# Kernel tuning notes

Hardware: AMD Instinct MI355X
Metric: run time of the kernel (lower is better)

Reference implementation:

```python
import jax, jax.numpy as jnp
import numpy as np

# normalization module stand-ins (simple monotone scalings, as in the repo they
# are fixed elementwise rescalings of the raw quantities)
def norm_local_x(n):
    return n

def norm_unit_contraction(c):
    return c

def norm_local_N(N):
    return jnp.log1p(N.astype(jnp.float32))

norm_TNG_radii = norm_local_x
norm_local_v = norm_local_x
norm_local_v0 = norm_local_x

EPS = 1e-5


def setup_inputs() -> dict:
    key = jax.random.key(0)
    ks = jax.random.split(key, 12)
    B, T, ND, KB = 2, 1024, 256, 3
    K_IN, H, L = 19, 128, 128
    x0 = 0.3 * jax.random.normal(ks[0], (B, T, 3), dtype=jnp.float32)
    # DM positions in local frame, |x| must stay < 1.05 (assert in original)
    x = jax.random.uniform(ks[1], (B, T, ND, 3), dtype=jnp.float32) - 0.5
    N = jax.random.randint(ks[2], (B, T), 1, 512, dtype=jnp.int32)
    basis = jax.random.normal(ks[3], (B, KB, 3), dtype=jnp.float32)
    v = jax.random.normal(ks[4], (B, T, ND, 3), dtype=jnp.float32)
    P200c = 0.5 + jax.random.uniform(ks[5], (B,), dtype=jnp.float32)
    s = 0.1
    W0 = s * jax.random.normal(ks[6], (K_IN, H - 1), dtype=jnp.float32)
    b0 = jnp.zeros((H - 1,), jnp.float32)
    W1 = s * jax.random.normal(ks[7], (H, H), dtype=jnp.float32)
    b1 = jnp.zeros((H,), jnp.float32)
    W2 = s * jax.random.normal(ks[8], (H, L), dtype=jnp.float32)
    b2 = jnp.zeros((L,), jnp.float32)
    return {"x0": x0, "x": x, "N": N, "basis": basis, "v": v, "P200c": P200c,
            "W0": W0, "b0": b0, "W1": W1, "b1": b1, "W2": W2, "b2": b2}


def create_scalars(x0, x, N, basis, v):
    B, T, ND, _ = x.shape
    # velocities relative to local mean (halo -> local frame)
    v0 = jnp.mean(v, axis=2)                      # [B,T,3]
    vc = v - v0[:, :, None, :]                    # [B,T,ND,3]

    x_norm = jnp.linalg.norm(x, axis=-1, keepdims=True) + EPS     # [B,T,ND,1]
    xu = x / x_norm
    x0_norm = jnp.linalg.norm(x0, axis=-1, keepdims=True) + EPS   # [B,T,1]
    x0u = x0 / x0_norm
    v0_norm = jnp.linalg.norm(v0, axis=-1, keepdims=True) + EPS   # [B,T,1]
    v0u = v0 / v0_norm
    v_norm = jnp.linalg.norm(vc, axis=-1, keepdims=True) + EPS    # [B,T,ND,1]
    vu = vc / v_norm

    bc = lambda a: jnp.broadcast_to(a[:, :, None, :], (B, T, ND, a.shape[-1]))

    feats = [
        norm_local_x(x_norm),                                          # |x| [1]
        norm_unit_contraction(jnp.einsum('btnd,bkd->btnk', xu, basis)),# x.basis [3]
        jnp.broadcast_to(norm_local_N(N)[:, :, None, None], (B, T, ND, 1)),  # N [1]
        bc(norm_TNG_radii(x0_norm)),                                   # |x0| [1]
        bc(norm_unit_contraction(jnp.einsum('btd,bkd->btk', x0u, basis))),  # x0.basis [3]
        bc(norm_local_v0(v0_norm)),                                    # |v0| [1]
        bc(norm_unit_contraction(jnp.einsum('btd,bkd->btk', v0u, basis))),  # v0.basis [3]
        bc(norm_unit_contraction(jnp.sum(x0u * v0u, axis=-1, keepdims=True))),  # x0.v0 [1]
        norm_local_v(v_norm),                                          # |v| [1]
        norm_unit_contraction(jnp.einsum('btnd,bkd->btnk', vu, basis)),# v.basis [3]
        norm_unit_contraction(jnp.sum(xu * vu, axis=-1, keepdims=True)),  # x.v [1]
    ]
    return jnp.concatenate(feats, axis=-1)  # [B,T,ND,19]


def reference(x0, x, N, basis, v, P200c, W0, b0, W1, b1, W2, b2):
    scalars = create_scalars(x0, x, N, basis, v)          # [B,T,ND,19]
    h = jax.nn.leaky_relu(scalars @ W0 + b0)              # [B,T,ND,H-1]
    h = jnp.mean(h, axis=2)                               # pool -> [B,T,H-1]
    h = jnp.concatenate([h, norm_local_N(N)[..., None]], axis=-1)  # [B,T,H]
    h = jax.nn.leaky_relu(h @ W1 + b1)                    # [B,T,H]
    out = h @ W2 + b2                                     # [B,T,Nlatent]
    return (1.0 / P200c)[:, None, None] * out
```

## Files before the change

kernel.cpp:

```cpp
#include <hip/hip_runtime.h>
#include <hip/hip_bf16.h>
#include <math.h>

#define EPSV 1e-5f
#define HD   128
#define AROW 40
#define WROW 40

typedef __attribute__((ext_vector_type(8))) short bf16x8;
typedef __attribute__((ext_vector_type(4))) float f32x4;

__global__ __launch_bounds__(256, 2) void net_fused(
    const float* __restrict__ x0g, const float* __restrict__ xg,
    const int*   __restrict__ Ng,  const float* __restrict__ basisg,
    const float* __restrict__ vg,  const float* __restrict__ Pg,
    const float* __restrict__ W0,  const float* __restrict__ b0,
    const float* __restrict__ W1,  const float* __restrict__ b1,
    const float* __restrict__ W2,  const float* __restrict__ b2,
    float* __restrict__ out, int Tn, int NDn)
{
    __shared__ __align__(16) __hip_bfloat16 SA[256 * AROW];
    __shared__ __align__(16) __hip_bfloat16 Wt1[128 * WROW];
    __shared__ __align__(16) __hip_bfloat16 Wt2[128 * WROW];
    __shared__ float cvec[HD];
    __shared__ float part[4][HD];
    __shared__ float hvec[HD];
    __shared__ float h1vec[HD];
    __shared__ float tailred[2][HD];
    __shared__ float vred[4][3];

    const int bt   = blockIdx.x;
    const int b    = bt / Tn;
    const int tid  = threadIdx.x;
    const int lane = tid & 63;
    const int wave = tid >> 6;

    const long pbase = ((long)bt * NDn + tid) * 3;
    const float xi0 = xg[pbase+0], xi1 = xg[pbase+1], xi2 = xg[pbase+2];
    const float vi0 = vg[pbase+0], vi1 = vg[pbase+1], vi2 = vg[pbase+2];

    float s0 = vi0, s1 = vi1, s2 = vi2;
    #pragma unroll
    for (int off = 32; off > 0; off >>= 1) {
        s0 += __shfl_down(s0, off);
        s1 += __shfl_down(s1, off);
        s2 += __shfl_down(s2, off);
    }
    if (lane == 0) { vred[wave][0] = s0; vred[wave][1] = s1; vred[wave][2] = s2; }

    {
        const int RV[9] = {0, 1, 2, 3, 14, 15, 16, 17, 18};
        if (tid < 128) {
            const int n = tid;
            __hip_bfloat16* w1 = &Wt1[n * WROW];
            __hip_bfloat16* w2 = &Wt2[n * WROW];
            const __hip_bfloat16 z16 = __float2bfloat16(0.0f);
            #pragma unroll
            for (int kk = 0; kk < 9; ++kk) {
                const float wv = (n < 127) ? W0[RV[kk] * 127 + n] : 0.0f;
                const __hip_bfloat16 hi = __float2bfloat16(wv);
                const __hip_bfloat16 lo = __float2bfloat16(wv - __bfloat162float(hi));
                w1[kk] = hi;  w1[16 + kk] = hi;
                w2[kk] = lo;  w2[16 + kk] = lo;
            }
            #pragma unroll
            for (int kk = 9; kk < 16; ++kk) {
                w1[kk] = z16;  w1[kk + 16] = z16;
                w2[kk] = z16;  w2[kk + 16] = z16;
            }
        }
    }
    __syncthreads();

    const float inv_nd = 1.0f / (float)NDn;
    const float v00 = (vred[0][0]+vred[1][0]+vred[2][0]+vred[3][0]) * inv_nd;
    const float v01 = (vred[0][1]+vred[1][1]+vred[2][1]+vred[3][1]) * inv_nd;
    const float v02 = (vred[0][2]+vred[1][2]+vred[2][2]+vred[3][2]) * inv_nd;

    const float p0 = x0g[bt*3+0], p1 = x0g[bt*3+1], p2 = x0g[bt*3+2];
    float bas[3][3];
    #pragma unroll
    for (int k = 0; k < 3; ++k)
        #pragma unroll
        for (int c = 0; c < 3; ++c)
            bas[k][c] = basisg[(b*3 + k)*3 + c];

    const float x0n  = sqrtf(p0*p0 + p1*p1 + p2*p2) + EPSV;
    const float ix0n = 1.0f / x0n;
    const float x0u0 = p0*ix0n, x0u1 = p1*ix0n, x0u2 = p2*ix0n;

    const float v0n  = sqrtf(v00*v00 + v01*v01 + v02*v02) + EPSV;
    const float iv0n = 1.0f / v0n;
    const float v0u0 = v00*iv0n, v0u1 = v01*iv0n, v0u2 = v02*iv0n;

    const float logN = log1pf((float)Ng[bt]);

    if (tid < 128) {
        float c = 0.0f;
        if (tid < 127) {
            float fc[10];
            fc[0] = logN;
            fc[1] = x0n;
            fc[2] = x0u0*bas[0][0] + x0u1*bas[0][1] + x0u2*bas[0][2];
            fc[3] = x0u0*bas[1][0] + x0u1*bas[1][1] + x0u2*bas[1][2];
            fc[4] = x0u0*bas[2][0] + x0u1*bas[2][1] + x0u2*bas[2][2];
            fc[5] = v0n;
            fc[6] = v0u0*bas[0][0] + v0u1*bas[0][1] + v0u2*bas[0][2];
            fc[7] = v0u0*bas[1][0] + v0u1*bas[1][1] + v0u2*bas[1][2];
            fc[8] = v0u0*bas[2][0] + v0u1*bas[2][1] + v0u2*bas[2][2];
            fc[9] = x0u0*v0u0 + x0u1*v0u1 + x0u2*v0u2;
            c = b0[tid];
            #pragma unroll
            for (int i = 0; i < 10; ++i)
                c = fmaf(fc[i], W0[(4 + i) * 127 + tid], c);
        }
        cvec[tid] = c;
    }

    {
        const float xn  = sqrtf(xi0*xi0 + xi1*xi1 + xi2*xi2) + EPSV;
        const float ixn = 1.0f / xn;
        const float xu0 = xi0*ixn, xu1 = xi1*ixn, xu2 = xi2*ixn;

        const float c0 = vi0 - v00, c1 = vi1 - v01, c2 = vi2 - v02;
        const float vn  = sqrtf(c0*c0 + c1*c1 + c2*c2) + EPSV;
        const float ivn = 1.0f / vn;
        const float vu0 = c0*ivn, vu1 = c1*ivn, vu2 = c2*ivn;

        float f[9];
        f[0] = xn;
        f[1] = xu0*bas[0][0] + xu1*bas[0][1] + xu2*bas[0][2];
        f[2] = xu0*bas[1][0] + xu1*bas[1][1] + xu2*bas[1][2];
        f[3] = xu0*bas[2][0] + xu1*bas[2][1] + xu2*bas[2][2];
        f[4] = vn;
        f[5] = vu0*bas[0][0] + vu1*bas[0][1] + vu2*bas[0][2];
        f[6] = vu0*bas[1][0] + vu1*bas[1][1] + vu2*bas[1][2];
        f[7] = vu0*bas[2][0] + vu1*bas[2][1] + vu2*bas[2][2];
        f[8] = xu0*vu0 + xu1*vu1 + xu2*vu2;

        __hip_bfloat16* Ar = &SA[tid * AROW];
        const __hip_bfloat16 z16 = __float2bfloat16(0.0f);
        #pragma unroll
        for (int kk = 0; kk < 9; ++kk) {
            const __hip_bfloat16 hi = __float2bfloat16(f[kk]);
            Ar[kk]      = hi;
            Ar[16 + kk] = __float2bfloat16(f[kk] - __bfloat162float(hi));
        }
        #pragma unroll
        for (int kk = 9; kk < 16; ++kk) {
            Ar[kk]      = z16;
            Ar[kk + 16] = z16;
        }
    }
    __syncthreads();

    {
        const int quad = lane >> 4;
        const int lm   = lane & 15;

        bf16x8 bf1[8], bf2[8];
        float  cl[8];
        #pragma unroll
        for (int nt = 0; nt < 8; ++nt) {
            bf1[nt] = *reinterpret_cast<const bf16x8*>(&Wt1[(nt*16 + lm) * WROW + quad*8]);
            bf2[nt] = *reinterpret_cast<const bf16x8*>(&Wt2[(nt*16 + lm) * WROW + quad*8]);
            cl[nt]  = cvec[nt*16 + lm];
        }

        float pooled[8];
        #pragma unroll
        for (int nt = 0; nt < 8; ++nt) pooled[nt] = 0.0f;

        const f32x4 zero = {0.f, 0.f, 0.f, 0.f};
        #pragma unroll
        for (int mt = 0; mt < 4; ++mt) {
            const int particle = wave*64 + mt*16 + lm;
            const bf16x8 af = *reinterpret_cast<const bf16x8*>(&SA[particle * AROW + quad*8]);
            #pragma unroll
            for (int nt = 0; nt < 8; ++nt) {
                f32x4 acc = __builtin_amdgcn_mfma_f32_16x16x32_bf16(af, bf1[nt], zero, 0, 0, 0);
                acc = __builtin_amdgcn_mfma_f32_16x16x32_bf16(af, bf2[nt], acc, 0, 0, 0);
                float t = 0.0f;
                #pragma unroll
                for (int r = 0; r < 4; ++r) {
                    const float d = acc[r] + cl[nt];
                    t += fmaxf(d, 0.01f*d);
                }
                pooled[nt] += t;
            }
        }
        #pragma unroll
        for (int nt = 0; nt < 8; ++nt) {
            pooled[nt] += __shfl_xor(pooled[nt], 16);
            pooled[nt] += __shfl_xor(pooled[nt], 32);
        }
        if (lane < 16) {
            #pragma unroll
            for (int nt = 0; nt < 8; ++nt)
                part[wave][nt*16 + lane] = pooled[nt];
        }
    }
    __syncthreads();

    if (tid < HD) {
        const float p = part[0][tid] + part[1][tid] + part[2][tid] + part[3][tid];
        hvec[tid] = (tid < 127) ? p * inv_nd : logN;
    }
    __syncthreads();

    {
        const int j    = tid & 127;
        const int half = tid >> 7;
        const int kb   = half * 64;
        float a = 0.0f;
        #pragma unroll 8
        for (int k = 0; k < 64; ++k) a = fmaf(hvec[kb + k], W1[(kb + k)*HD + j], a);
        tailred[half][j] = a;
    }
    __syncthreads();
    if (tid < HD) {
        const float a = b1[tid] + tailred[0][tid] + tailred[1][tid];
        h1vec[tid] = fmaxf(a, 0.01f*a);
    }
    __syncthreads();

    {
        const int j    = tid & 127;
        const int half = tid >> 7;
        const int kb   = half * 64;
        float a = 0.0f;
        #pragma unroll 8
        for (int k = 0; k < 64; ++k) a = fmaf(h1vec[kb + k], W2[(kb + k)*HD + j], a);
        tailred[half][j] = a;
    }
    __syncthreads();
    if (tid < HD) {
        const float a = b2[tid] + tailred[0][tid] + tailred[1][tid];
        out[(long)bt * HD + tid] = a / Pg[b];
    }
}

extern "C" void kernel_launch(void* const* d_in, const int* in_sizes, int n_in,
                              void* d_out, int out_size, void* d_ws, size_t ws_size,
                              hipStream_t stream) {
    const float* x0    = (const float*)d_in[0];
    const float* x     = (const float*)d_in[1];
    const int*   N     = (const int*)  d_in[2];
    const float* basis = (const float*)d_in[3];
    const float* v     = (const float*)d_in[4];
    const float* P200c = (const float*)d_in[5];
    const float* W0    = (const float*)d_in[6];
    const float* b0    = (const float*)d_in[7];
    const float* W1    = (const float*)d_in[8];
    const float* b1    = (const float*)d_in[9];
    const float* W2    = (const float*)d_in[10];
    const float* b2    = (const float*)d_in[11];
    float* out = (float*)d_out;

    const int B  = in_sizes[5];
    const int T  = in_sizes[2] / B;
    const int ND = in_sizes[1] / (in_sizes[2] * 3);

    dim3 grid(B * T), block(256);
    hipLaunchKernelGGL(net_fused, grid, block, 0, stream,
                       x0, x, N, basis, v, P200c, W0, b0, W1, b1, W2, b2,
                       out, T, ND);
}
```

Measured before the change: 119.0 us.

## Vectorize LDS row writes, single-pass tail matvecs, raise occupancy bound

```diff
diff --git a/kernel.cpp b/kernel.cpp
--- a/kernel.cpp
+++ b/kernel.cpp
@@ -10,7 +10,7 @@
 typedef __attribute__((ext_vector_type(8))) short bf16x8;
 typedef __attribute__((ext_vector_type(4))) float f32x4;
 
-__global__ __launch_bounds__(256, 2) void net_fused(
+__global__ __launch_bounds__(256, 3) void net_fused(
     const float* __restrict__ x0g, const float* __restrict__ xg,
     const int*   __restrict__ Ng,  const float* __restrict__ basisg,
     const float* __restrict__ vg,  const float* __restrict__ Pg,
@@ -26,7 +26,6 @@
     __shared__ float part[4][HD];
     __shared__ float hvec[HD];
     __shared__ float h1vec[HD];
-    __shared__ float tailred[2][HD];
     __shared__ float vred[4][3];
 
     const int bt   = blockIdx.x;
@@ -48,27 +47,30 @@
     }
     if (lane == 0) { vred[wave][0] = s0; vred[wave][1] = s1; vred[wave][2] = s2; }
 
-    {
+    if (tid < 128) {
         const int RV[9] = {0, 1, 2, 3, 14, 15, 16, 17, 18};
-        if (tid < 128) {
-            const int n = tid;
-            __hip_bfloat16* w1 = &Wt1[n * WROW];
-            __hip_bfloat16* w2 = &Wt2[n * WROW];
-            const __hip_bfloat16 z16 = __float2bfloat16(0.0f);
+        __hip_bfloat16 r1[32], r2[32];
+        #pragma unroll
+        for (int kk = 0; kk < 32; ++kk) {
+            r1[kk] = __float2bfloat16(0.0f);
+            r2[kk] = __float2bfloat16(0.0f);
+        }
+        if (tid < 127) {
             #pragma unroll
             for (int kk = 0; kk < 9; ++kk) {
-                const float wv = (n < 127) ? W0[RV[kk] * 127 + n] : 0.0f;
+                const float wv = W0[RV[kk] * 127 + tid];
                 const __hip_bfloat16 hi = __float2bfloat16(wv);
                 const __hip_bfloat16 lo = __float2bfloat16(wv - __bfloat162float(hi));
-                w1[kk] = hi;  w1[16 + kk] = hi;
-                w2[kk] = lo;  w2[16 + kk] = lo;
+                r1[kk] = hi;  r1[16 + kk] = hi;
+                r2[kk] = lo;  r2[16 + kk] = lo;
             }
-            #pragma unroll
-            for (int kk = 9; kk < 16; ++kk) {
-                w1[kk] = z16;  w1[kk + 16] = z16;
-                w2[kk] = z16;  w2[kk + 16] = z16;
-            }
-        }
+        }
+        bf16x8* d1 = reinterpret_cast<bf16x8*>(&Wt1[tid * WROW]);
+        bf16x8* d2 = reinterpret_cast<bf16x8*>(&Wt2[tid * WROW]);
+        const bf16x8* s1v = reinterpret_cast<const bf16x8*>(r1);
+        const bf16x8* s2v = reinterpret_cast<const bf16x8*>(r2);
+        d1[0]=s1v[0]; d1[1]=s1v[1]; d1[2]=s1v[2]; d1[3]=s1v[3];
+        d2[0]=s2v[0]; d2[1]=s2v[1]; d2[2]=s2v[2]; d2[3]=s2v[3];
     }
     __syncthreads();
 
@@ -138,19 +140,18 @@
         f[7] = vu0*bas[2][0] + vu1*bas[2][1] + vu2*bas[2][2];
         f[8] = xu0*vu0 + xu1*vu1 + xu2*vu2;
 
-        __hip_bfloat16* Ar = &SA[tid * AROW];
-        const __hip_bfloat16 z16 = __float2bfloat16(0.0f);
+        __hip_bfloat16 row[32];
+        #pragma unroll
+        for (int kk = 0; kk < 32; ++kk) row[kk] = __float2bfloat16(0.0f);
         #pragma unroll
         for (int kk = 0; kk < 9; ++kk) {
             const __hip_bfloat16 hi = __float2bfloat16(f[kk]);
-            Ar[kk]      = hi;
-            Ar[16 + kk] = __float2bfloat16(f[kk] - __bfloat162float(hi));
-        }
-        #pragma unroll
-        for (int kk = 9; kk < 16; ++kk) {
-            Ar[kk]      = z16;
-            Ar[kk + 16] = z16;
-        }
+            row[kk]      = hi;
+            row[16 + kk] = __float2bfloat16(f[kk] - __bfloat162float(hi));
+        }
+        bf16x8* dst = reinterpret_cast<bf16x8*>(&SA[tid * AROW]);
+        const bf16x8* src = reinterpret_cast<const bf16x8*>(row);
+        dst[0] = src[0]; dst[1] = src[1]; dst[2] = src[2]; dst[3] = src[3];
     }
     __syncthreads();
 
@@ -174,19 +175,17 @@
         const f32x4 zero = {0.f, 0.f, 0.f, 0.f};
         #pragma unroll
         for (int mt = 0; mt < 4; ++mt) {
-            const int particle = wave*64 + mt*16 + lm;
-            const bf16x8 af = *reinterpret_cast<const bf16x8*>(&SA[particle * AROW + quad*8]);
+            const bf16x8 af = *reinterpret_cast<const bf16x8*>(
+                &SA[(wave*64 + mt*16 + lm) * AROW + quad*8]);
             #pragma unroll
             for (int nt = 0; nt < 8; ++nt) {
                 f32x4 acc = __builtin_amdgcn_mfma_f32_16x16x32_bf16(af, bf1[nt], zero, 0, 0, 0);
                 acc = __builtin_amdgcn_mfma_f32_16x16x32_bf16(af, bf2[nt], acc, 0, 0, 0);
-                float t = 0.0f;
                 #pragma unroll
                 for (int r = 0; r < 4; ++r) {
                     const float d = acc[r] + cl[nt];
-                    t += fmaxf(d, 0.01f*d);
+                    pooled[nt] += fmaxf(d, 0.01f*d);
                 }
-                pooled[nt] += t;
             }
         }
         #pragma unroll
@@ -208,34 +207,20 @@
     }
     __syncthreads();
 
-    {
-        const int j    = tid & 127;
-        const int half = tid >> 7;
-        const int kb   = half * 64;
-        float a = 0.0f;
-        #pragma unroll 8
-        for (int k = 0; k < 64; ++k) a = fmaf(hvec[kb + k], W1[(kb + k)*HD + j], a);
-        tailred[half][j] = a;
-    }
-    __syncthreads();
     if (tid < HD) {
-        const float a = b1[tid] + tailred[0][tid] + tailred[1][tid];
+        float a = b1[tid];
+        #pragma unroll 16
+        for (int k = 0; k < HD; ++k)
+            a = fmaf(hvec[k], W1[k*HD + tid], a);
         h1vec[tid] = fmaxf(a, 0.01f*a);
     }
     __syncthreads();
 
-    {
-        const int j    = tid & 127;
-        const int half = tid >> 7;
-        const int kb   = half * 64;
-        float a = 0.0f;
-        #pragma unroll 8
-        for (int k = 0; k < 64; ++k) a = fmaf(h1vec[kb + k], W2[(kb + k)*HD + j], a);
-        tailred[half][j] = a;
-    }
-    __syncthreads();
     if (tid < HD) {
-        const float a = b2[tid] + tailred[0][tid] + tailred[1][tid];
+        float a = b2[tid];
+        #pragma unroll 16
+        for (int k = 0; k < HD; ++k)
+            a = fmaf(h1vec[k], W2[k*HD + tid], a);
         out[(long)bt * HD + tid] = a / Pg[b];
     }
 }
@@ -261,8 +246,7 @@
     const int T  = in_sizes[2] / B;
     const int ND = in_sizes[1] / (in_sizes[2] * 3);
 
-    dim3 grid(B * T), block(256);
-    hipLaunchKernelGGL(net_fused, grid, block, 0, stream,
+    hipLaunchKernelGGL(net_fused, dim3(B * T), dim3(256), 0, stream,
                        x0, x, N, basis, v, P200c, W0, b0, W1, b1, W2, b2,
                        out, T, ND);
 }
```

After: 113.2 us. 1.05x faster.
